# Kernel tuning notes

Hardware: AMD Instinct MI355X
Metric: run time of the kernel (lower is better)

## Reference

```python
import jax, jax.numpy as jnp
import numpy as np

D_MODEL = 768
N_HEADS = 12
D_K = D_MODEL // N_HEADS
WINDOW = 256
NEG_INF = -1e30


def setup_inputs() -> dict:
    key = jax.random.key(0)
    ks = jax.random.split(key, 9)
    s = 0.02
    x = jax.random.normal(ks[0], (2, 2048, D_MODEL), dtype=jnp.float32)
    Wq = jax.random.normal(ks[1], (D_MODEL, D_MODEL), dtype=jnp.float32) * s
    bq = jnp.zeros((D_MODEL,), dtype=jnp.float32)
    Wk = jax.random.normal(ks[2], (D_MODEL, D_MODEL), dtype=jnp.float32) * s
    bk = jnp.zeros((D_MODEL,), dtype=jnp.float32)
    Wv = jax.random.normal(ks[3], (D_MODEL, D_MODEL), dtype=jnp.float32) * s
    bv = jnp.zeros((D_MODEL,), dtype=jnp.float32)
    Wo = jax.random.normal(ks[4], (D_MODEL, D_MODEL), dtype=jnp.float32) * s
    bo = jnp.zeros((D_MODEL,), dtype=jnp.float32)
    return {"x": x, "Wq": Wq, "bq": bq, "Wk": Wk, "bk": bk,
            "Wv": Wv, "bv": bv, "Wo": Wo, "bo": bo}


def _window_mask(seq_len: int) -> jnp.ndarray:
    # Faithful to _apply_sliding_window_attention: scores are reshaped into
    # (nw, ws, nw, ws) windows and a causal tril is applied broadcast over BOTH
    # window indices => position (q, k) allowed iff (q % ws) >= (k % ws).
    # (seq_len here is a multiple of WINDOW, so pad/slice is a no-op.)
    if seq_len <= WINDOW:
        q = jnp.arange(seq_len)
        return q[:, None] >= jnp.arange(seq_len)[None, :]
    qmod = jnp.arange(seq_len) % WINDOW
    return qmod[:, None] >= qmod[None, :]


def reference(x, Wq, bq, Wk, bk, Wv, bv, Wo, bo):
    B, S, _ = x.shape
    # torch nn.Linear: y = x @ W.T + b
    q = (x @ Wq.T + bq).reshape(B, S, N_HEADS, D_K).transpose(0, 2, 1, 3)
    k = (x @ Wk.T + bk).reshape(B, S, N_HEADS, D_K).transpose(0, 2, 1, 3)
    v = (x @ Wv.T + bv).reshape(B, S, N_HEADS, D_K).transpose(0, 2, 1, 3)
    scores = jnp.einsum('bhqd,bhkd->bhqk', q, k) / jnp.sqrt(jnp.float32(D_K))
    mask = _window_mask(S)  # [S, S] bool
    scores = jnp.where(mask[None, None, :, :], scores, NEG_INF)
    probs = jax.nn.softmax(scores, axis=-1)  # dropout p=0 (eval)
    out = jnp.einsum('bhqk,bhkd->bhqd', probs, v)
    out = out.transpose(0, 2, 1, 3).reshape(B, S, D_MODEL)
    return out @ Wo.T + bo
```

## Files before the change

kernel.cpp:

```cpp
#include <hip/hip_runtime.h>

typedef unsigned short u16;
typedef unsigned int u32;
typedef unsigned long long u64;
typedef __attribute__((ext_vector_type(8))) short bfrag;
typedef __attribute__((ext_vector_type(4))) float f32x4;
typedef __attribute__((ext_vector_type(16))) float f32x16;
typedef __attribute__((ext_vector_type(4))) u32 u32x4;

#define QSCALE 0.18033688f

__device__ __forceinline__ u16 f2bf(float f) {
    unsigned u = __float_as_uint(f);
    u += 0x7FFFu + ((u >> 16) & 1u);
    return (u16)(u >> 16);
}

__device__ __forceinline__ u32 cvt_pk_bf16(float lo, float hi) {
    u32 r;
    asm("v_cvt_pk_bf16_f32 %0, %1, %2" : "=v"(r) : "v"(lo), "v"(hi));
    return r;
}

__device__ __forceinline__ void glds16(const void* g, void* l) {
    __builtin_amdgcn_global_load_lds((__attribute__((address_space(1))) void*)g,
                                     (__attribute__((address_space(3))) void*)l,
                                     16, 0, 0);
}

__device__ __forceinline__ f32x16 mfma32(bfrag a, bfrag b, f32x16 c) {
    return __builtin_amdgcn_mfma_f32_32x32x16_bf16(a, b, c, 0, 0, 0);
}

#define WAIT_VM4()  asm volatile("s_waitcnt vmcnt(4)" ::: "memory")
#define WAIT_VM3()  asm volatile("s_waitcnt vmcnt(3)" ::: "memory")
#define WAIT_VM0()  asm volatile("s_waitcnt vmcnt(0)" ::: "memory")
#define BAR()       __builtin_amdgcn_s_barrier()
#define SCHED_FENCE() __builtin_amdgcn_sched_barrier(0)
#define PRIO(n)     __builtin_amdgcn_s_setprio(n)

__global__ __launch_bounds__(256) void convert_all(
    const float* __restrict__ x, const float* __restrict__ wq,
    const float* __restrict__ wk, const float* __restrict__ wv,
    const float* __restrict__ wo,
    u16* __restrict__ xb, u16* __restrict__ wqb, u16* __restrict__ wkb,
    u16* __restrict__ wvb, u16* __restrict__ wob) {
    const int XV = (2 * 2048 * 768) / 4;
    const int WV = (768 * 768) / 4;
    int i = blockIdx.x * 256 + threadIdx.x;
    if (i >= XV + 4 * WV) return;
    const float4* src; u16* dst; int off;
    if (i < XV) { src = (const float4*)x; dst = xb; off = i; }
    else {
        int j = i - XV; int z = j / WV; off = j - z * WV;
        src = (const float4*)(z == 0 ? wq : z == 1 ? wk : z == 2 ? wv : wo);
        dst = (z == 0 ? wqb : z == 1 ? wkb : z == 2 ? wvb : wob);
    }
    float4 v = src[off];
    u64 pk = (u64)f2bf(v.x)
        | ((u64)f2bf(v.y) << 16)
        | ((u64)f2bf(v.z) << 32)
        | ((u64)f2bf(v.w) << 48);
    *(u64*)(dst + off * 4) = pk;
}

__device__ __forceinline__ void gemm_core(
    const u16* __restrict__ A, const u16* __restrict__ Bw, int m0,
    u16* a_lds, u16* b_lds, f32x4 acc[4][4]) {
    const int t = threadIdx.x;
    const int w = t >> 6, lane = t & 63, ln = lane & 15, lh = lane >> 4;
    const int wr = w >> 1, wc = w & 1;

    const int row0 = t >> 2;
    const int u0 = (t & 3) ^ ((row0 >> 1) & 3);
    const int row1 = row0 + 64;
    const int u1 = (t & 3) ^ ((row1 >> 1) & 3);
    const u16* ga0 = A + (m0 + row0) * 768 + u0 * 8;
    const u16* ga1 = A + (m0 + row1) * 768 + u1 * 8;
    const u16* gb0 = Bw + row0 * 768 + u0 * 8;
    const u16* gb1 = Bw + row1 * 768 + u1 * 8;
    u16* la = a_lds + w * 512;
    u16* lb = b_lds + w * 512;

    auto STAGE = [&](int k0, int bi) {
        glds16(ga0 + k0, la + bi * 4096);
        glds16(ga1 + k0, la + bi * 4096 + 2048);
        glds16(gb0 + k0, lb + bi * 4096);
        glds16(gb1 + k0, lb + bi * 4096 + 2048);
    };

    STAGE(0, 0);
    int cur = 0;
    for (int k0 = 0; k0 < 768; k0 += 32) {
        if (k0 + 32 < 768) {
            STAGE(k0 + 32, cur ^ 1);
            WAIT_VM4();
        } else {
            WAIT_VM0();
        }
        BAR();
        SCHED_FENCE();
        const u16* ab = a_lds + cur * 4096;
        const u16* bb = b_lds + cur * 4096;
        bfrag aF[4], bF[4];
#pragma unroll
        for (int i = 0; i < 4; i++) {
            int ra = wr * 64 + i * 16 + ln;
            aF[i] = *(const bfrag*)(ab + ra * 32 + ((lh ^ ((ra >> 1) & 3)) * 8));
            int rb = wc * 64 + i * 16 + ln;
            bF[i] = *(const bfrag*)(bb + rb * 32 + ((lh ^ ((rb >> 1) & 3)) * 8));
        }
#pragma unroll
        for (int i = 0; i < 4; i++)
#pragma unroll
            for (int j = 0; j < 4; j++)
                acc[i][j] = __builtin_amdgcn_mfma_f32_16x16x32_bf16(
                    aF[i], bF[j], acc[i][j], 0, 0, 0);
        SCHED_FENCE();
        BAR();
        cur ^= 1;
    }
}

__global__ __launch_bounds__(256) void gemm_qkv(
    const u16* __restrict__ xb,
    const u16* __restrict__ wqb, const u16* __restrict__ wkb, const u16* __restrict__ wvb,
    const float* __restrict__ bq, const float* __restrict__ bk, const float* __restrict__ bv,
    u16* __restrict__ q_ws, u16* __restrict__ k_ws, u16* __restrict__ vt_ws) {
    __shared__ __align__(16) u16 smem[16384];
    u16* a_lds = smem;
    u16* b_lds = smem + 8192;
    const int m0 = blockIdx.x * 128;
    const int z = blockIdx.y / 6, nb = blockIdx.y % 6;
    const u16* Bw = (z == 0 ? wqb : z == 1 ? wkb : wvb) + nb * 128 * 768;
    const float* bias = (z == 0 ? bq : z == 1 ? bk : bv);

    f32x4 acc[4][4] = {};
    gemm_core(xb, Bw, m0, a_lds, b_lds, acc);

    const int t = threadIdx.x, w = t >> 6, lane = t & 63, ln = lane & 15, lh = lane >> 4;
    const int wr = w >> 1, wc = w & 1;
    if (z == 2) {
        __syncthreads();
        char* T = (char*)smem;
#pragma unroll
        for (int j = 0; j < 4; j++) {
            int nt = wc * 64 + j * 16 + ln;
            float bb = bias[nb * 128 + nt];
#pragma unroll
            for (int i = 0; i < 4; i++) {
                int m0t = wr * 64 + i * 16 + lh * 4;
                u64 pk = (u64)f2bf(acc[i][j][0] + bb)
                    | ((u64)f2bf(acc[i][j][1] + bb) << 16)
                    | ((u64)f2bf(acc[i][j][2] + bb) << 32)
                    | ((u64)f2bf(acc[i][j][3] + bb) << 48);
                int off = nt * 256 + ((m0t * 2) ^ ((nt & 15) << 4));
                *(u64*)(T + off) = pk;
            }
        }
        __syncthreads();
        const int b = m0 >> 11, s0 = m0 & 2047;
#pragma unroll
        for (int c = 0; c < 8; c++) {
            int g = c * 256 + t;
            int nt = g >> 4, mc = (g & 15) * 8;
            int off = nt * 256 + ((mc * 2) ^ ((nt & 15) << 4));
            u32x4 v = *(const u32x4*)(T + off);
            int nl = nb * 128 + nt;
            int h = nl >> 6, d = nl & 63;
            *(u32x4*)(vt_ws + ((size_t)((b * 12 + h) * 64 + d)) * 2048 + s0 + mc) = v;
        }
    } else {
        u16* dst = (z == 0 ? q_ws : k_ws);
        const float sc = (z == 0) ? QSCALE : 1.0f;
#pragma unroll
        for (int j = 0; j < 4; j++) {
            int nl = nb * 128 + wc * 64 + j * 16 + ln;
            int h = nl >> 6, d = nl & 63;
            float bb = bias[nl];
#pragma unroll
            for (int i = 0; i < 4; i++)
#pragma unroll
                for (int r = 0; r < 4; r++) {
                    int m = m0 + wr * 64 + i * 16 + lh * 4 + r;
                    int b = m >> 11, s = m & 2047;
                    dst[((size_t)((b * 12 + h) * 2048 + s)) * 64 + d] = f2bf((acc[i][j][r] + bb) * sc);
                }
        }
    }
}

__global__ __launch_bounds__(256) void gemm_out64(
    const u16* __restrict__ ob, const u16* __restrict__ wob,
    const float* __restrict__ bo, float* __restrict__ out) {
    __shared__ __align__(16) u16 a_lds[2 * 64 * 32];
    __shared__ __align__(16) u16 b_lds[2 * 128 * 32];
    const int m0 = blockIdx.x * 64, n0 = blockIdx.y * 128;
    const int t = threadIdx.x;
    const int w = t >> 6, lane = t & 63, ln = lane & 15, lh = lane >> 4;
    const int wr = w >> 1, wc = w & 1;

    const int rowA = t >> 2;
    const int uA = (t & 3) ^ ((rowA >> 1) & 3);
    const int rowB1 = rowA + 64;
    const int uB1 = (t & 3) ^ ((rowB1 >> 1) & 3);
    const u16* ga  = ob + (m0 + rowA) * 768 + uA * 8;
    const u16* gb0 = wob + (n0 + rowA) * 768 + uA * 8;
    const u16* gb1 = wob + (n0 + rowB1) * 768 + uB1 * 8;
    u16* la = a_lds + w * 512;
    u16* lb = b_lds + w * 512;

    auto STAGE = [&](int k0, int bi) {
        glds16(ga + k0, la + bi * 2048);
        glds16(gb0 + k0, lb + bi * 4096);
        glds16(gb1 + k0, lb + bi * 4096 + 2048);
    };

    f32x4 acc[2][4] = {};
    STAGE(0, 0);
    int cur = 0;
    for (int k0 = 0; k0 < 768; k0 += 32) {
        if (k0 + 32 < 768) {
            STAGE(k0 + 32, cur ^ 1);
            WAIT_VM3();
        } else {
            WAIT_VM0();
        }
        BAR();
        SCHED_FENCE();
        const u16* ab = a_lds + cur * 2048;
        const u16* bb = b_lds + cur * 4096;
        bfrag aF[2], bF[4];
#pragma unroll
        for (int i = 0; i < 2; i++) {
            int ra = wr * 32 + i * 16 + ln;
            aF[i] = *(const bfrag*)(ab + ra * 32 + ((lh ^ ((ra >> 1) & 3)) * 8));
        }
#pragma unroll
        for (int j = 0; j < 4; j++) {
            int rb = wc * 64 + j * 16 + ln;
            bF[j] = *(const bfrag*)(bb + rb * 32 + ((lh ^ ((rb >> 1) & 3)) * 8));
        }
#pragma unroll
        for (int i = 0; i < 2; i++)
#pragma unroll
            for (int j = 0; j < 4; j++)
                acc[i][j] = __builtin_amdgcn_mfma_f32_16x16x32_bf16(
                    aF[i], bF[j], acc[i][j], 0, 0, 0);
        SCHED_FENCE();
        BAR();
        cur ^= 1;
    }
#pragma unroll
    for (int j = 0; j < 4; j++) {
        int n = n0 + wc * 64 + j * 16 + ln;
        float bb = bo[n];
#pragma unroll
        for (int i = 0; i < 2; i++)
#pragma unroll
            for (int r = 0; r < 4; r++) {
                int m = m0 + wr * 32 + i * 16 + lh * 4 + r;
                out[m * 768 + n] = acc[i][j][r] + bb;
            }
    }
}

__global__ __launch_bounds__(256) void attn8(
    const u16* __restrict__ q_ws, const u16* __restrict__ k_ws,
    const u16* __restrict__ vt_ws, u16* __restrict__ o_ws,
    u16* __restrict__ po_ws, float* __restrict__ l_ws) {
    __shared__ __align__(16) u16 k_lds[2][64 * 64];
    __shared__ __align__(16) u16 v_lds[2][64 * 64];

    const int t = threadIdx.x, w = t >> 6, l = t & 63, lq = l & 31, H = l >> 5;
    int id = blockIdx.x;
    int bh8 = id & 7, idq = id >> 3;
    int bhq = idq % 3, pg = idq / 3;
    int t7, rem;
    if (pg < 16)      { t7 = 7 - (pg >> 3); rem = pg & 7; }
    else if (pg < 28) { int u = pg - 16; t7 = 5 - u / 6; rem = u % 6; }
    else if (pg < 36) { int u = pg - 28; t7 = 3 - (u >> 2); rem = u & 3; }
    else              { int u = pg - 36; t7 = 1 - (u >> 1); rem = u & 1; }
    const int np = (t7 + 2) >> 1;
    const int quad = rem / np, piece = rem - quad * np;
    const int bh = bhq * 8 + bh8;
    const int ti = quad * 4 + w;
    const int tile = t7 + 8 * ti;
    const int qw0 = tile * 32;

    const u16* Qb = q_ws + (size_t)bh * 2048 * 64;
    const u16* Kb = k_ws + (size_t)bh * 2048 * 64;
    const u16* Vt = vt_ws + (size_t)bh * 64 * 2048;

    const int lqp = (lq & 19) | ((lq & 4) << 1) | ((lq & 8) >> 1);
    const int ksw = lqp & 7;
    const int vsw = lq & 7;

    bfrag qF[4];
#pragma unroll
    for (int kd = 0; kd < 4; kd++)
        qF[kd] = *(const bfrag*)(Qb + (size_t)(qw0 + lq) * 64 + kd * 16 + H * 8);

    const f32x16 Z = {};
    f32x16 O0 = Z, O1 = Z;
    float lsum = 0.f;

    const int skey = t >> 3;
    const int su = (t & 7) ^ (skey & 7);

    auto STAGE = [&](int k0, int bi) {
        glds16(Kb + (size_t)(k0 + skey) * 64 + su * 8,        k_lds[bi] + w * 512);
        glds16(Kb + (size_t)(k0 + skey + 32) * 64 + su * 8,   k_lds[bi] + 2048 + w * 512);
        glds16(Vt + (size_t)skey * 2048 + k0 + su * 8,        v_lds[bi] + w * 512);
        glds16(Vt + (size_t)(skey + 32) * 2048 + k0 + su * 8, v_lds[bi] + 2048 + w * 512);
    };

    int gp0 = piece * 8;
    int win = gp0 / np, pb = gp0 - win * np;
    STAGE(win * 256 + pb * 64, 0);

    for (int j = 0; j < 8; ++j) {
        int winn = win, pbn = pb + 1;
        if (pbn == np) { pbn = 0; winn = win + 1; }
        if (j < 7) {
            STAGE(winn * 256 + pbn * 64, (j + 1) & 1);
            WAIT_VM4();
        } else {
            WAIT_VM0();
        }
        BAR();
        SCHED_FENCE();

        const int cb = 2 * pb;
        const bool c1 = (cb + 1) <= t7, d0 = (cb == t7), d1 = (cb + 1 == t7);
        const u16* kl = k_lds[j & 1];
        const u16* vl = v_lds[j & 1];

        PRIO(1);
        f32x16 s0, s1;
        {
            bfrag kf = *(const bfrag*)(kl + lqp * 64 + ((H) ^ ksw) * 8);
            s0 = mfma32(kf, qF[0], Z);
#pragma unroll
            for (int kd = 1; kd < 4; kd++) {
                bfrag k2 = *(const bfrag*)(kl + lqp * 64 + ((kd * 2 + H) ^ ksw) * 8);
                s0 = mfma32(k2, qF[kd], s0);
            }
        }
        if (c1) {
            bfrag kf = *(const bfrag*)(kl + (32 + lqp) * 64 + ((H) ^ ksw) * 8);
            s1 = mfma32(kf, qF[0], Z);
#pragma unroll
            for (int kd = 1; kd < 4; kd++) {
                bfrag k2 = *(const bfrag*)(kl + (32 + lqp) * 64 + ((kd * 2 + H) ^ ksw) * 8);
                s1 = mfma32(k2, qF[kd], s1);
            }
        }
        PRIO(0);

        float ps = 0.f;
        u32 pkA[8], pkB[8];
        if (d0) {
#pragma unroll
            for (int r2 = 0; r2 < 16; r2++) {
                int ka = (r2 & 3) + 4 * ((r2 >> 2) & 1) + 16 * (r2 >> 3) + 8 * H;
                if (ka > lq) s0[r2] = -1e30f;
            }
        }
#pragma unroll
        for (int i = 0; i < 8; i++) {
            float a = exp2f(s0[2 * i]), b2 = exp2f(s0[2 * i + 1]);
            ps += a + b2; pkA[i] = cvt_pk_bf16(a, b2);
        }
        if (c1) {
            if (d1) {
#pragma unroll
                for (int r2 = 0; r2 < 16; r2++) {
                    int ka = (r2 & 3) + 4 * ((r2 >> 2) & 1) + 16 * (r2 >> 3) + 8 * H;
                    if (ka > lq) s1[r2] = -1e30f;
                }
            }
#pragma unroll
            for (int i = 0; i < 8; i++) {
                float a = exp2f(s1[2 * i]), b2 = exp2f(s1[2 * i + 1]);
                ps += a + b2; pkB[i] = cvt_pk_bf16(a, b2);
            }
        }
        lsum += ps;

        PRIO(1);
        {
            u32x4 a0 = {pkA[0], pkA[1], pkA[2], pkA[3]};
            u32x4 a1 = {pkA[4], pkA[5], pkA[6], pkA[7]};
            bfrag A0 = __builtin_bit_cast(bfrag, a0);
            bfrag A1 = __builtin_bit_cast(bfrag, a1);
            bfrag v00 = *(const bfrag*)(vl + lq * 64 + ((H) ^ vsw) * 8);
            bfrag v01 = *(const bfrag*)(vl + (32 + lq) * 64 + ((H) ^ vsw) * 8);
            bfrag v10 = *(const bfrag*)(vl + lq * 64 + ((2 + H) ^ vsw) * 8);
            bfrag v11 = *(const bfrag*)(vl + (32 + lq) * 64 + ((2 + H) ^ vsw) * 8);
            O0 = mfma32(A0, v00, O0);
            O1 = mfma32(A0, v01, O1);
            O0 = mfma32(A1, v10, O0);
            O1 = mfma32(A1, v11, O1);
        }
        if (c1) {
            u32x4 a0 = {pkB[0], pkB[1], pkB[2], pkB[3]};
            u32x4 a1 = {pkB[4], pkB[5], pkB[6], pkB[7]};
            bfrag A0 = __builtin_bit_cast(bfrag, a0);
            bfrag A1 = __builtin_bit_cast(bfrag, a1);
            bfrag v00 = *(const bfrag*)(vl + lq * 64 + ((4 + H) ^ vsw) * 8);
            bfrag v01 = *(const bfrag*)(vl + (32 + lq) * 64 + ((4 + H) ^ vsw) * 8);
            bfrag v10 = *(const bfrag*)(vl + lq * 64 + ((6 + H) ^ vsw) * 8);
            bfrag v11 = *(const bfrag*)(vl + (32 + lq) * 64 + ((6 + H) ^ vsw) * 8);
            O0 = mfma32(A0, v00, O0);
            O1 = mfma32(A0, v01, O1);
            O0 = mfma32(A1, v10, O0);
            O1 = mfma32(A1, v11, O1);
        }
        PRIO(0);
        SCHED_FENCE();
        BAR();
        win = winn; pb = pbn;
    }

    float lsT = lsum + __shfl_xor(lsum, 32);
    if (np == 1) {
        float linv = 1.f / lsT;
        const int b = bh / 12, h = bh % 12;
#pragma unroll
        for (int r2 = 0; r2 < 16; r2++) {
            int row = (r2 & 3) + 8 * (r2 >> 2) + 4 * H;
            float fr = __shfl(linv, row);
            size_t base = ((size_t)(b * 2048 + qw0 + row)) * 768 + h * 64;
            o_ws[base + lq] = f2bf(O0[r2] * fr);
            o_ws[base + 32 + lq] = f2bf(O1[r2] * fr);
        }
    } else {
        const int cum8[8] = {0, 8, 16, 32, 48, 72, 96, 128};
        size_t pidx = (size_t)bh * 160 + cum8[t7] + ti * np + piece;
        u16* po = po_ws + pidx * 2048;
#pragma unroll
        for (int r2 = 0; r2 < 16; r2++) {
            int row = (r2 & 3) + 8 * (r2 >> 2) + 4 * H;
            po[row * 64 + lq] = f2bf(O0[r2]);
            po[row * 64 + 32 + lq] = f2bf(O1[r2]);
        }
        if (l < 32) l_ws[pidx * 32 + lq] = lsT;
    }
}

__global__ __launch_bounds__(256) void combine_o(
    const u16* __restrict__ po_ws, const float* __restrict__ l_ws,
    u16* __restrict__ o_ws) {
    int id = blockIdx.x;
    int bh8 = id & 7, idq = id >> 3;
    int bhq = idq % 3, r = idq / 3;
    int bh = bhq * 8 + bh8;
    int t7 = 2 + (r >> 3), ti = r & 7;
    int tile = t7 + 8 * ti;
    int np = (t7 + 2) >> 1;
    const int cum8[8] = {0, 8, 16, 32, 48, 72, 96, 128};
    size_t base = (size_t)bh * 160 + cum8[t7] + ti * np;
    int t = threadIdx.x;
    int q = t >> 3, d8 = (t & 7) * 8;
    float acc[8] = {0.f, 0.f, 0.f, 0.f, 0.f, 0.f, 0.f, 0.f};
    float lt = 0.f;
    for (int i = 0; i < np; i++) {
        lt += l_ws[(base + i) * 32 + q];
        bfrag v = *(const bfrag*)(po_ws + (base + i) * 2048 + q * 64 + d8);
#pragma unroll
        for (int e = 0; e < 8; e++)
            acc[e] += __uint_as_float(((u32)(u16)v[e]) << 16);
    }
    float inv = 1.f / lt;
    u32x4 pkv;
#pragma unroll
    for (int e = 0; e < 4; e++)
        pkv[e] = cvt_pk_bf16(acc[2 * e] * inv, acc[2 * e + 1] * inv);
    int b = bh / 12, h = bh % 12;
    size_t dst = ((size_t)(b * 2048 + tile * 32 + q)) * 768 + h * 64 + d8;
    *(u32x4*)(o_ws + dst) = pkv;
}

extern "C" void kernel_launch(void* const* d_in, const int* in_sizes, int n_in,
                              void* d_out, int out_size, void* d_ws, size_t ws_size,
                              hipStream_t stream) {
    const float* x  = (const float*)d_in[0];
    const float* Wq = (const float*)d_in[1];
    const float* bq = (const float*)d_in[2];
    const float* Wk = (const float*)d_in[3];
    const float* bk = (const float*)d_in[4];
    const float* Wv = (const float*)d_in[5];
    const float* bv = (const float*)d_in[6];
    const float* Wo = (const float*)d_in[7];
    const float* bo = (const float*)d_in[8];
    float* out = (float*)d_out;

    char* p = (char*)d_ws;
    u16*   q_ws  = (u16*)(p + 0);
    u16*   k_ws  = (u16*)(p + 6291456);
    u16*   vt_ws = (u16*)(p + 12582912);
    u16*   po_ws = (u16*)(p + 18874368);
    u16*   xb    = (u16*)(p + 18874368);
    u16*   wqb   = (u16*)(p + 25165824);
    u16*   wkb   = (u16*)(p + 26345472);
    u16*   wvb   = (u16*)(p + 27525120);
    float* l_ws  = (float*)(p + 34603008);
    u16*   wob   = (u16*)(p + 35094528);
    u16*   o_ws  = (u16*)(p + 36274176);

    convert_all<<<5376, 256, 0, stream>>>(x, Wq, Wk, Wv, Wo, xb, wqb, wkb, wvb, wob);
    gemm_qkv<<<dim3(32, 18), 256, 0, stream>>>(xb, wqb, wkb, wvb, bq, bk, bv, q_ws, k_ws, vt_ws);
    attn8<<<dim3(960), 256, 0, stream>>>(q_ws, k_ws, vt_ws, o_ws, po_ws, l_ws);
    combine_o<<<dim3(1152), 256, 0, stream>>>(po_ws, l_ws, o_ws);
    gemm_out64<<<dim3(64, 6), 256, 0, stream>>>(o_ws, wob, bo, out);
}
```

Baseline: 90.95 us.

## Process two query tiles per wave in attention to reuse staged K/V

Result: slower. 100.4 us (+10.3%).

```diff
diff --git a/kernel.cpp b/kernel.cpp
--- a/kernel.cpp
+++ b/kernel.cpp
@@ -190,12 +190,9 @@
     }
 }
 
-__global__ __launch_bounds__(256) void gemm_out64(
-    const u16* __restrict__ ob, const u16* __restrict__ wob,
-    const float* __restrict__ bo, float* __restrict__ out) {
-    __shared__ __align__(16) u16 a_lds[2 * 64 * 32];
-    __shared__ __align__(16) u16 b_lds[2 * 128 * 32];
-    const int m0 = blockIdx.x * 64, n0 = blockIdx.y * 128;
+__device__ __forceinline__ void gemm_core64(
+    const u16* __restrict__ A, const u16* __restrict__ Bw, int m0,
+    u16* a_lds, u16* b_lds, f32x4 acc[2][4]) {
     const int t = threadIdx.x;
     const int w = t >> 6, lane = t & 63, ln = lane & 15, lh = lane >> 4;
     const int wr = w >> 1, wc = w & 1;
@@ -204,9 +201,9 @@
     const int uA = (t & 3) ^ ((rowA >> 1) & 3);
     const int rowB1 = rowA + 64;
     const int uB1 = (t & 3) ^ ((rowB1 >> 1) & 3);
-    const u16* ga  = ob + (m0 + rowA) * 768 + uA * 8;
-    const u16* gb0 = wob + (n0 + rowA) * 768 + uA * 8;
-    const u16* gb1 = wob + (n0 + rowB1) * 768 + uB1 * 8;
+    const u16* ga  = A + (m0 + rowA) * 768 + uA * 8;
+    const u16* gb0 = Bw + rowA * 768 + uA * 8;
+    const u16* gb1 = Bw + rowB1 * 768 + uB1 * 8;
     u16* la = a_lds + w * 512;
     u16* lb = b_lds + w * 512;
 
@@ -216,7 +213,6 @@
         glds16(gb1 + k0, lb + bi * 4096 + 2048);
     };
 
-    f32x4 acc[2][4] = {};
     STAGE(0, 0);
     int cur = 0;
     for (int k0 = 0; k0 < 768; k0 += 32) {
@@ -251,6 +247,18 @@
         BAR();
         cur ^= 1;
     }
+}
+
+__global__ __launch_bounds__(256) void gemm_out64(
+    const u16* __restrict__ ob, const u16* __restrict__ wob,
+    const float* __restrict__ bo, float* __restrict__ out) {
+    __shared__ __align__(16) u16 a_lds[2 * 64 * 32];
+    __shared__ __align__(16) u16 b_lds[2 * 128 * 32];
+    const int m0 = blockIdx.x * 64, n0 = blockIdx.y * 128;
+    f32x4 acc[2][4] = {};
+    gemm_core64(ob, wob + n0 * 768, m0, a_lds, b_lds, acc);
+    const int t = threadIdx.x, w = t >> 6, lane = t & 63, ln = lane & 15, lh = lane >> 4;
+    const int wr = w >> 1, wc = w & 1;
 #pragma unroll
     for (int j = 0; j < 4; j++) {
         int n = n0 + wc * 64 + j * 16 + ln;
@@ -265,7 +273,7 @@
     }
 }
 
-__global__ __launch_bounds__(256) void attn8(
+__global__ __launch_bounds__(256) void attn9(
     const u16* __restrict__ q_ws, const u16* __restrict__ k_ws,
     const u16* __restrict__ vt_ws, u16* __restrict__ o_ws,
     u16* __restrict__ po_ws, float* __restrict__ l_ws) {
@@ -276,17 +284,20 @@
     int id = blockIdx.x;
     int bh8 = id & 7, idq = id >> 3;
     int bhq = idq % 3, pg = idq / 3;
-    int t7, rem;
-    if (pg < 16)      { t7 = 7 - (pg >> 3); rem = pg & 7; }
-    else if (pg < 28) { int u = pg - 16; t7 = 5 - u / 6; rem = u % 6; }
-    else if (pg < 36) { int u = pg - 28; t7 = 3 - (u >> 2); rem = u & 3; }
-    else              { int u = pg - 36; t7 = 1 - (u >> 1); rem = u & 1; }
+    int t7, piece;
+    if (pg < 4)       { t7 = 7; piece = pg; }
+    else if (pg < 8)  { t7 = 6; piece = pg - 4; }
+    else if (pg < 11) { t7 = 5; piece = pg - 8; }
+    else if (pg < 14) { t7 = 4; piece = pg - 11; }
+    else if (pg < 16) { t7 = 3; piece = pg - 14; }
+    else if (pg < 18) { t7 = 2; piece = pg - 16; }
+    else if (pg < 19) { t7 = 1; piece = 0; }
+    else              { t7 = 0; piece = 0; }
     const int np = (t7 + 2) >> 1;
-    const int quad = rem / np, piece = rem - quad * np;
     const int bh = bhq * 8 + bh8;
-    const int ti = quad * 4 + w;
-    const int tile = t7 + 8 * ti;
-    const int qw0 = tile * 32;
+    const int tiA = w, tiB = w + 4;
+    const int qw0a = (t7 + 8 * tiA) * 32;
+    const int qw0b = (t7 + 8 * tiB) * 32;
 
     const u16* Qb = q_ws + (size_t)bh * 2048 * 64;
     const u16* Kb = k_ws + (size_t)bh * 2048 * 64;
@@ -296,14 +307,16 @@
     const int ksw = lqp & 7;
     const int vsw = lq & 7;
 
-    bfrag qF[4];
-#pragma unroll
-    for (int kd = 0; kd < 4; kd++)
-        qF[kd] = *(const bfrag*)(Qb + (size_t)(qw0 + lq) * 64 + kd * 16 + H * 8);
+    bfrag qFa[4], qFb[4];
+#pragma unroll
+    for (int kd = 0; kd < 4; kd++) {
+        qFa[kd] = *(const bfrag*)(Qb + (size_t)(qw0a + lq) * 64 + kd * 16 + H * 8);
+        qFb[kd] = *(const bfrag*)(Qb + (size_t)(qw0b + lq) * 64 + kd * 16 + H * 8);
+    }
 
     const f32x16 Z = {};
-    f32x16 O0 = Z, O1 = Z;
-    float lsum = 0.f;
+    f32x16 O0a = Z, O1a = Z, O0b = Z, O1b = Z;
+    float lsa = 0.f, lsb = 0.f;
 
     const int skey = t >> 3;
     const int su = (t & 7) ^ (skey & 7);
@@ -337,115 +350,193 @@
         const u16* vl = v_lds[j & 1];
 
         PRIO(1);
-        f32x16 s0, s1;
+        f32x16 s0a, s1a, s0b, s1b;
         {
             bfrag kf = *(const bfrag*)(kl + lqp * 64 + ((H) ^ ksw) * 8);
-            s0 = mfma32(kf, qF[0], Z);
+            s0a = mfma32(kf, qFa[0], Z);
+            s0b = mfma32(kf, qFb[0], Z);
 #pragma unroll
             for (int kd = 1; kd < 4; kd++) {
                 bfrag k2 = *(const bfrag*)(kl + lqp * 64 + ((kd * 2 + H) ^ ksw) * 8);
-                s0 = mfma32(k2, qF[kd], s0);
+                s0a = mfma32(k2, qFa[kd], s0a);
+                s0b = mfma32(k2, qFb[kd], s0b);
             }
         }
         if (c1) {
             bfrag kf = *(const bfrag*)(kl + (32 + lqp) * 64 + ((H) ^ ksw) * 8);
-            s1 = mfma32(kf, qF[0], Z);
+            s1a = mfma32(kf, qFa[0], Z);
+            s1b = mfma32(kf, qFb[0], Z);
 #pragma unroll
             for (int kd = 1; kd < 4; kd++) {
                 bfrag k2 = *(const bfrag*)(kl + (32 + lqp) * 64 + ((kd * 2 + H) ^ ksw) * 8);
-                s1 = mfma32(k2, qF[kd], s1);
+                s1a = mfma32(k2, qFa[kd], s1a);
+                s1b = mfma32(k2, qFb[kd], s1b);
             }
         }
         PRIO(0);
 
-        float ps = 0.f;
-        u32 pkA[8], pkB[8];
-        if (d0) {
-#pragma unroll
-            for (int r2 = 0; r2 < 16; r2++) {
-                int ka = (r2 & 3) + 4 * ((r2 >> 2) & 1) + 16 * (r2 >> 3) + 8 * H;
-                if (ka > lq) s0[r2] = -1e30f;
-            }
-        }
-#pragma unroll
-        for (int i = 0; i < 8; i++) {
-            float a = exp2f(s0[2 * i]), b2 = exp2f(s0[2 * i + 1]);
-            ps += a + b2; pkA[i] = cvt_pk_bf16(a, b2);
-        }
-        if (c1) {
-            if (d1) {
+        bfrag v0[4], v1[4];
+        {
+            v0[0] = *(const bfrag*)(vl + lq * 64 + ((H) ^ vsw) * 8);
+            v1[0] = *(const bfrag*)(vl + (32 + lq) * 64 + ((H) ^ vsw) * 8);
+            v0[1] = *(const bfrag*)(vl + lq * 64 + ((2 + H) ^ vsw) * 8);
+            v1[1] = *(const bfrag*)(vl + (32 + lq) * 64 + ((2 + H) ^ vsw) * 8);
+            if (c1) {
+                v0[2] = *(const bfrag*)(vl + lq * 64 + ((4 + H) ^ vsw) * 8);
+                v1[2] = *(const bfrag*)(vl + (32 + lq) * 64 + ((4 + H) ^ vsw) * 8);
+                v0[3] = *(const bfrag*)(vl + lq * 64 + ((6 + H) ^ vsw) * 8);
+                v1[3] = *(const bfrag*)(vl + (32 + lq) * 64 + ((6 + H) ^ vsw) * 8);
+            }
+        }
+
+        {
+            float ps = 0.f;
+            u32 pkA[8], pkB[8];
+            if (d0) {
 #pragma unroll
                 for (int r2 = 0; r2 < 16; r2++) {
                     int ka = (r2 & 3) + 4 * ((r2 >> 2) & 1) + 16 * (r2 >> 3) + 8 * H;
-                    if (ka > lq) s1[r2] = -1e30f;
+                    if (ka > lq) s0a[r2] = -1e30f;
                 }
             }
 #pragma unroll
             for (int i = 0; i < 8; i++) {
-                float a = exp2f(s1[2 * i]), b2 = exp2f(s1[2 * i + 1]);
-                ps += a + b2; pkB[i] = cvt_pk_bf16(a, b2);
-            }
-        }
-        lsum += ps;
-
-        PRIO(1);
+                float a = exp2f(s0a[2 * i]), b2 = exp2f(s0a[2 * i + 1]);
+                ps += a + b2; pkA[i] = cvt_pk_bf16(a, b2);
+            }
+            if (c1) {
+                if (d1) {
+#pragma unroll
+                    for (int r2 = 0; r2 < 16; r2++) {
+                        int ka = (r2 & 3) + 4 * ((r2 >> 2) & 1) + 16 * (r2 >> 3) + 8 * H;
+                        if (ka > lq) s1a[r2] = -1e30f;
+                    }
+                }
+#pragma unroll
+                for (int i = 0; i < 8; i++) {
+                    float a = exp2f(s1a[2 * i]), b2 = exp2f(s1a[2 * i + 1]);
+                    ps += a + b2; pkB[i] = cvt_pk_bf16(a, b2);
+                }
+            }
+            lsa += ps;
+            PRIO(1);
+            {
+                u32x4 a0 = {pkA[0], pkA[1], pkA[2], pkA[3]};
+                u32x4 a1 = {pkA[4], pkA[5], pkA[6], pkA[7]};
+                bfrag A0 = __builtin_bit_cast(bfrag, a0);
+                bfrag A1 = __builtin_bit_cast(bfrag, a1);
+                O0a = mfma32(A0, v0[0], O0a);
+                O1a = mfma32(A0, v1[0], O1a);
+                O0a = mfma32(A1, v0[1], O0a);
+                O1a = mfma32(A1, v1[1], O1a);
+            }
+            if (c1) {
+                u32x4 a0 = {pkB[0], pkB[1], pkB[2], pkB[3]};
+                u32x4 a1 = {pkB[4], pkB[5], pkB[6], pkB[7]};
+                bfrag A0 = __builtin_bit_cast(bfrag, a0);
+                bfrag A1 = __builtin_bit_cast(bfrag, a1);
+                O0a = mfma32(A0, v0[2], O0a);
+                O1a = mfma32(A0, v1[2], O1a);
+                O0a = mfma32(A1, v0[3], O0a);
+                O1a = mfma32(A1, v1[3], O1a);
+            }
+            PRIO(0);
+        }
+
         {
-            u32x4 a0 = {pkA[0], pkA[1], pkA[2], pkA[3]};
-            u32x4 a1 = {pkA[4], pkA[5], pkA[6], pkA[7]};
-            bfrag A0 = __builtin_bit_cast(bfrag, a0);
-            bfrag A1 = __builtin_bit_cast(bfrag, a1);
-            bfrag v00 = *(const bfrag*)(vl + lq * 64 + ((H) ^ vsw) * 8);
-            bfrag v01 = *(const bfrag*)(vl + (32 + lq) * 64 + ((H) ^ vsw) * 8);
-            bfrag v10 = *(const bfrag*)(vl + lq * 64 + ((2 + H) ^ vsw) * 8);
-            bfrag v11 = *(const bfrag*)(vl + (32 + lq) * 64 + ((2 + H) ^ vsw) * 8);
-            O0 = mfma32(A0, v00, O0);
-            O1 = mfma32(A0, v01, O1);
-            O0 = mfma32(A1, v10, O0);
-            O1 = mfma32(A1, v11, O1);
-        }
-        if (c1) {
-            u32x4 a0 = {pkB[0], pkB[1], pkB[2], pkB[3]};
-            u32x4 a1 = {pkB[4], pkB[5], pkB[6], pkB[7]};
-            bfrag A0 = __builtin_bit_cast(bfrag, a0);
-            bfrag A1 = __builtin_bit_cast(bfrag, a1);
-            bfrag v00 = *(const bfrag*)(vl + lq * 64 + ((4 + H) ^ vsw) * 8);
-            bfrag v01 = *(const bfrag*)(vl + (32 + lq) * 64 + ((4 + H) ^ vsw) * 8);
-            bfrag v10 = *(const bfrag*)(vl + lq * 64 + ((6 + H) ^ vsw) * 8);
-            bfrag v11 = *(const bfrag*)(vl + (32 + lq) * 64 + ((6 + H) ^ vsw) * 8);
-            O0 = mfma32(A0, v00, O0);
-            O1 = mfma32(A0, v01, O1);
-            O0 = mfma32(A1, v10, O0);
-            O1 = mfma32(A1, v11, O1);
-        }
-        PRIO(0);
+            float ps = 0.f;
+            u32 pkA[8], pkB[8];
+            if (d0) {
+#pragma unroll
+                for (int r2 = 0; r2 < 16; r2++) {
+                    int ka = (r2 & 3) + 4 * ((r2 >> 2) & 1) + 16 * (r2 >> 3) + 8 * H;
+                    if (ka > lq) s0b[r2] = -1e30f;
+                }
+            }
+#pragma unroll
+            for (int i = 0; i < 8; i++) {
+                float a = exp2f(s0b[2 * i]), b2 = exp2f(s0b[2 * i + 1]);
+                ps += a + b2; pkA[i] = cvt_pk_bf16(a, b2);
+            }
+            if (c1) {
+                if (d1) {
+#pragma unroll
+                    for (int r2 = 0; r2 < 16; r2++) {
+                        int ka = (r2 & 3) + 4 * ((r2 >> 2) & 1) + 16 * (r2 >> 3) + 8 * H;
+                        if (ka > lq) s1b[r2] = -1e30f;
+                    }
+                }
+#pragma unroll
+                for (int i = 0; i < 8; i++) {
+                    float a = exp2f(s1b[2 * i]), b2 = exp2f(s1b[2 * i + 1]);
+                    ps += a + b2; pkB[i] = cvt_pk_bf16(a, b2);
+                }
+            }
+            lsb += ps;
+            PRIO(1);
+            {
+                u32x4 a0 = {pkA[0], pkA[1], pkA[2], pkA[3]};
+                u32x4 a1 = {pkA[4], pkA[5], pkA[6], pkA[7]};
+                bfrag A0 = __builtin_bit_cast(bfrag, a0);
+                bfrag A1 = __builtin_bit_cast(bfrag, a1);
+                O0b = mfma32(A0, v0[0], O0b);
+                O1b = mfma32(A0, v1[0], O1b);
+                O0b = mfma32(A1, v0[1], O0b);
+                O1b = mfma32(A1, v1[1], O1b);
+            }
+            if (c1) {
+                u32x4 a0 = {pkB[0], pkB[1], pkB[2], pkB[3]};
+                u32x4 a1 = {pkB[4], pkB[5], pkB[6], pkB[7]};
+                bfrag A0 = __builtin_bit_cast(bfrag, a0);
+                bfrag A1 = __builtin_bit_cast(bfrag, a1);
+                O0b = mfma32(A0, v0[2], O0b);
+                O1b = mfma32(A0, v1[2], O1b);
+                O0b = mfma32(A1, v0[3], O0b);
+                O1b = mfma32(A1, v1[3], O1b);
+            }
+            PRIO(0);
+        }
+
         SCHED_FENCE();
         BAR();
         win = winn; pb = pbn;
     }
 
-    float lsT = lsum + __shfl_xor(lsum, 32);
+    const int cum8[8] = {0, 8, 16, 32, 48, 72, 96, 128};
+    const int b = bh / 12, h = bh % 12;
+    float lsTa = lsa + __shfl_xor(lsa, 32);
+    float lsTb = lsb + __shfl_xor(lsb, 32);
     if (np == 1) {
-        float linv = 1.f / lsT;
-        const int b = bh / 12, h = bh % 12;
+        float liva = 1.f / lsTa, livb = 1.f / lsTb;
 #pragma unroll
         for (int r2 = 0; r2 < 16; r2++) {
             int row = (r2 & 3) + 8 * (r2 >> 2) + 4 * H;
-            float fr = __shfl(linv, row);
-            size_t base = ((size_t)(b * 2048 + qw0 + row)) * 768 + h * 64;
-            o_ws[base + lq] = f2bf(O0[r2] * fr);
-            o_ws[base + 32 + lq] = f2bf(O1[r2] * fr);
+            float fra = __shfl(liva, row);
+            float frb = __shfl(livb, row);
+            size_t ba = ((size_t)(b * 2048 + qw0a + row)) * 768 + h * 64;
+            size_t bb2 = ((size_t)(b * 2048 + qw0b + row)) * 768 + h * 64;
+            o_ws[ba + lq] = f2bf(O0a[r2] * fra);
+            o_ws[ba + 32 + lq] = f2bf(O1a[r2] * fra);
+            o_ws[bb2 + lq] = f2bf(O0b[r2] * frb);
+            o_ws[bb2 + 32 + lq] = f2bf(O1b[r2] * frb);
         }
     } else {
-        const int cum8[8] = {0, 8, 16, 32, 48, 72, 96, 128};
-        size_t pidx = (size_t)bh * 160 + cum8[t7] + ti * np + piece;
-        u16* po = po_ws + pidx * 2048;
+        size_t pa = (size_t)bh * 160 + cum8[t7] + tiA * np + piece;
+        size_t pbx = (size_t)bh * 160 + cum8[t7] + tiB * np + piece;
+        u16* poa = po_ws + pa * 2048;
+        u16* pob = po_ws + pbx * 2048;
 #pragma unroll
         for (int r2 = 0; r2 < 16; r2++) {
             int row = (r2 & 3) + 8 * (r2 >> 2) + 4 * H;
-            po[row * 64 + lq] = f2bf(O0[r2]);
-            po[row * 64 + 32 + lq] = f2bf(O1[r2]);
-        }
-        if (l < 32) l_ws[pidx * 32 + lq] = lsT;
+            poa[row * 64 + lq] = f2bf(O0a[r2]);
+            poa[row * 64 + 32 + lq] = f2bf(O1a[r2]);
+            pob[row * 64 + lq] = f2bf(O0b[r2]);
+            pob[row * 64 + 32 + lq] = f2bf(O1b[r2]);
+        }
+        if (l < 32) {
+            l_ws[pa * 32 + lq] = lsTa;
+            l_ws[pbx * 32 + lq] = lsTb;
+        }
     }
 }
 
@@ -511,7 +602,7 @@
 
     convert_all<<<5376, 256, 0, stream>>>(x, Wq, Wk, Wv, Wo, xb, wqb, wkb, wvb, wob);
     gemm_qkv<<<dim3(32, 18), 256, 0, stream>>>(xb, wqb, wkb, wvb, bq, bk, bv, q_ws, k_ws, vt_ws);
-    attn8<<<dim3(960), 256, 0, stream>>>(q_ws, k_ws, vt_ws, o_ws, po_ws, l_ws);
+    attn9<<<dim3(480), 256, 0, stream>>>(q_ws, k_ws, vt_ws, o_ws, po_ws, l_ws);
     combine_o<<<dim3(1152), 256, 0, stream>>>(po_ws, l_ws, o_ws);
     gemm_out64<<<dim3(64, 6), 256, 0, stream>>>(o_ws, wob, bo, out);
 }
```
